# Optimization experiments

Hardware: AMD Instinct MI355X
Metric: run time of the kernel (lower is better)

The kernel has to match this reference:

```python
import jax, jax.numpy as jnp
import numpy as np

IMG_H = IMG_W = 640
NUM_CLASSES = 80
B = 8
NUM_ANCHORS = 76725
MAX_TOTAL = 200          # max_total_size == max_size_per_class
SCORE_TH = 0.5
IOU_TH = 0.5
K_CAND = 256             # per-class candidate pool for NMS (>= max survivors)
VARIANCES = jnp.asarray([0.1, 0.1, 0.2, 0.2], jnp.float32)


def _build_anchors(img_h, img_w):
    # RetinaNet AnchorBox: levels 3..7, 3 ratios x 3 scales, [cx, cy, w, h]
    ratios = [0.5, 1.0, 2.0]
    scales = [2.0 ** x for x in (0.0, 1.0 / 3.0, 2.0 / 3.0)]
    areas = [s * s for s in (32.0, 64.0, 128.0, 256.0, 512.0)]
    out = []
    for lvl, stride in enumerate([2 ** i for i in range(3, 8)]):
        dims = []
        for r in ratios:
            h = np.sqrt(areas[lvl] / r)
            w = areas[lvl] / h
            for s in scales:
                dims.append([w * s, h * s])
        dims = np.asarray(dims, np.float32)                      # [9,2]
        fh = int(np.ceil(img_h / stride)); fw = int(np.ceil(img_w / stride))
        rx = (np.arange(fw, dtype=np.float32) + 0.5) * stride
        ry = (np.arange(fh, dtype=np.float32) + 0.5) * stride
        cx, cy = np.meshgrid(rx, ry)
        centers = np.broadcast_to(np.stack([cx, cy], -1)[:, :, None, :], (fh, fw, 9, 2))
        d = np.broadcast_to(dims[None, None], (fh, fw, 9, 2))
        out.append(np.concatenate([centers, d], -1).reshape(-1, 4))
    return jnp.asarray(np.concatenate(out, 0))                   # [A,4]


def setup_inputs() -> dict:
    key = jax.random.key(0)
    k1, k2 = jax.random.split(key)
    box_pred = jax.random.normal(k1, (B, NUM_ANCHORS, 4), jnp.float32)
    cls_pred = jax.random.normal(k2, (B, NUM_ANCHORS, NUM_CLASSES), jnp.float32)
    anchor_boxes = _build_anchors(IMG_H, IMG_W)
    return {"box_pred": box_pred, "cls_pred": cls_pred, "anchor_boxes": anchor_boxes}


def _iou_one_vs_many(box, boxes):
    # box [4] vs boxes [K,4] in corner format
    lt = jnp.maximum(box[:2], boxes[:, :2])
    rb = jnp.minimum(box[2:], boxes[:, 2:])
    wh = jnp.maximum(rb - lt, 0.0)
    inter = wh[:, 0] * wh[:, 1]
    a1 = (box[2] - box[0]) * (box[3] - box[1])
    a2 = (boxes[:, 2] - boxes[:, 0]) * (boxes[:, 3] - boxes[:, 1])
    return inter / jnp.maximum(a1 + a2 - inter, 1e-8)


def _nms_keep(boxes, scores):
    # boxes [K,4] already sorted by descending score; greedy NMS
    eligible = scores > SCORE_TH
    idx = jnp.arange(K_CAND)

    def body(i, keep):
        iou = _iou_one_vs_many(boxes[i], boxes)
        suppress = (iou > IOU_TH) & (idx > i)
        return jnp.where(keep[i], keep & ~suppress, keep)

    keep = jax.lax.fori_loop(0, K_CAND, body, eligible)
    keep = keep & ((jnp.cumsum(keep) - 1) < MAX_TOTAL)           # max_size_per_class cap
    return keep


def _decode_and_nms(box_pred, cls_pred, anchor_boxes):
    scores_all = jax.nn.sigmoid(cls_pred)                        # [B,A,C]
    # decode: (dx,dy,dw,dh)*variances against [cx,cy,w,h] anchors
    d = box_pred * VARIANCES
    xy = d[..., :2] * anchor_boxes[None, :, 2:] + anchor_boxes[None, :, :2]
    wh = jnp.exp(d[..., 2:]) * anchor_boxes[None, :, 2:]
    boxes = jnp.concatenate([xy - 0.5 * wh, xy + 0.5 * wh], -1)  # [B,A,4] corners

    sc = jnp.swapaxes(scores_all, 1, 2)                          # [B,C,A]
    top_sc, top_idx = jax.lax.top_k(sc, K_CAND)                  # [B,C,K] sorted desc
    cand_boxes = jnp.take_along_axis(boxes[:, None], top_idx[..., None], axis=2)  # [B,C,K,4]

    keep = jax.lax.stop_gradient(jax.vmap(jax.vmap(_nms_keep))(cand_boxes, top_sc))  # [B,C,K]
    sel = jnp.where(keep, top_sc, -1.0)

    flat_sc = sel.reshape(B, -1)                                 # [B,C*K]
    flat_boxes = cand_boxes.reshape(B, -1, 4)
    flat_lbl = jnp.broadcast_to(jnp.arange(NUM_CLASSES)[None, :, None],
                                (B, NUM_CLASSES, K_CAND)).reshape(B, -1)

    fs, fi = jax.lax.top_k(flat_sc, MAX_TOTAL)                   # combine across classes
    out_boxes = jnp.take_along_axis(flat_boxes, fi[..., None], axis=1)
    out_lbl = jnp.take_along_axis(flat_lbl, fi, axis=1).astype(jnp.float32)
    valid = fs > 0.0                                             # pad invalid slots
    return (jnp.where(valid[..., None], out_boxes, 0.0),
            jnp.where(valid, fs, 0.0),
            jnp.where(valid, out_lbl, -1.0))


def reference(box_pred, cls_pred, anchor_boxes):
    return _decode_and_nms(box_pred, cls_pred, anchor_boxes)
```

## Files before the change

### kernel.cpp

```cpp
#include <hip/hip_runtime.h>
#include <math.h>
#include <stdint.h>

typedef unsigned long long u64;
typedef unsigned int u32;

#define NB 8
#define NA 76725
#define NC 80
#define KC 256
#define MAXT 200
#define CAP 2048
#define TCAP 1024
#define SELCAP 768
#define TAU 2.0f
#define TAU_STORE 2.5f
#define CHUNK 512
#define NCHUNK 150
#define BCAP 32
#define CSTRIDE 16

#define OFF_BUFA      0ull
#define OFF_CLASSLIST 5242880ull
#define OFF_CANDBOX   6553600ull
#define OFF_COUNTS    9175040ull

__device__ __forceinline__ void kf_proc(float4 v, int i, int a0,
                                        u64 (*bucket)[BCAP], u32* bcnt) {
  int a = a0 + i / (NC / 4);
  int c0 = (i % (NC / 4)) * 4;
  float vv[4] = {v.x, v.y, v.z, v.w};
#pragma unroll
  for (int j = 0; j < 4; j++) {
    if (vv[j] > TAU_STORE) {
      int c = c0 + j;
      u32 pos = atomicAdd(&bcnt[c], 1u);
      if (pos < BCAP)
        bucket[c][pos] = ((u64)__float_as_uint(vv[j]) << 32) | (u32)a;
    }
  }
}

__global__ __launch_bounds__(256) void kfilter(const float* __restrict__ cls,
                                               u64* __restrict__ bufA,
                                               u32* __restrict__ counts) {
  __shared__ u64 bucket[NC][BCAP];
  __shared__ u32 bcnt[NC];
  __shared__ u32 gbase[NC];
  __shared__ u32 pref[NC + 1];

  const int b = blockIdx.x / NCHUNK;
  const int ch = blockIdx.x % NCHUNK;
  const int tid = threadIdx.x;
  const int a0 = ch * CHUNK;
  const int aN = (NA - a0) < CHUNK ? (NA - a0) : CHUNK;

  for (int i = tid; i < NC; i += 256) bcnt[i] = 0;
  __syncthreads();

  const float4* p = (const float4*)(cls + ((size_t)b * NA + a0) * NC);
  const int n4 = aN * (NC / 4);
  for (int i0 = tid; i0 < n4; i0 += 2048) {
    float4 v[8];
    bool g[8];
#pragma unroll
    for (int u = 0; u < 8; u++) {
      g[u] = (i0 + u * 256) < n4;
      if (g[u]) v[u] = p[i0 + u * 256];
    }
#pragma unroll
    for (int u = 0; u < 8; u++)
      if (g[u]) kf_proc(v[u], i0 + u * 256, a0, bucket, bcnt);
  }
  __syncthreads();
  if (tid < NC) {
    u32 n = bcnt[tid];
    if (n > BCAP) n = BCAP;
    bcnt[tid] = n;
    gbase[tid] = atomicAdd(&counts[(b * NC + tid) * CSTRIDE], n);
  }
  __syncthreads();
  if (tid == 0) {
    u32 s = 0;
    for (int c = 0; c < NC; c++) { pref[c] = s; s += bcnt[c]; }
    pref[NC] = s;
  }
  __syncthreads();
  const int total = (int)pref[NC];
  for (int e = tid; e < total; e += 256) {
    int lo = 0, hi = NC;
    while (lo + 1 < hi) { int mid = (lo + hi) >> 1; if ((int)pref[mid] <= e) lo = mid; else hi = mid; }
    int c = lo;
    int loc = e - (int)pref[c];
    u32 gb = gbase[c] + (u32)loc;
    if (gb < TCAP)
      bufA[((size_t)(b * NC + c)) * TCAP + gb] = bucket[c][loc];
  }
}

__device__ __forceinline__ int logit_bin(u64 k) {
  float f = __uint_as_float((u32)(k >> 32));
  int bin = (int)(f * 170.0f);
  return bin < 0 ? 0 : (bin > 1023 ? 1023 : bin);
}

__device__ __forceinline__ bool iou_gt(float4 bi, float ai, float4 bj, float aj) {
  float lx = fmaxf(bi.x, bj.x), ly = fmaxf(bi.y, bj.y);
  float rx = fminf(bi.z, bj.z), ry = fminf(bi.w, bj.w);
  float wx = fmaxf(__fsub_rn(rx, lx), 0.0f);
  float wy = fmaxf(__fsub_rn(ry, ly), 0.0f);
  float inter = __fmul_rn(wx, wy);
  float uni = fmaxf(__fsub_rn(__fadd_rn(ai, aj), inter), 1e-8f);
  return __fdiv_rn(inter, uni) > 0.5f;
}

__global__ __launch_bounds__(256) void kselect(
    const float* __restrict__ cls, const float* __restrict__ boxp,
    const float* __restrict__ anc, const u64* __restrict__ bufA,
    const u32* __restrict__ counts, u64* __restrict__ classList,
    float4* __restrict__ candBox) {
  __shared__ __align__(16) char smem[24576];
  u64* sbuf = (u64*)smem;
  u64 (*scolT)[KC] = (u64(*)[KC])smem;
  float4* sBox = (float4*)(smem + 8192);
  float* sAr = (float*)(smem + 12288);
  u32* hist = (u32*)(smem + 16384);
  u64* sel = (u64*)(smem + 16384);
  u64* skey = (u64*)(smem + 22528);
  __shared__ u32 sRowAnyLo[4], sRowAnyHi[4];
  __shared__ int sNsel, sExtra, sSb;

  const int tid = threadIdx.x;
  const int bc = blockIdx.x;
  const int b = bc / NC, c = bc % NC;
  const u64* buf = bufA + (size_t)bc * TCAP;

  int cntT = (int)counts[bc * CSTRIDE];
  if (cntT > TCAP) cntT = TCAP;

  for (int i = tid; i < 1024; i += 256) hist[i] = 0;
  if (tid == 0) { sNsel = 0; sExtra = 0; }
  skey[tid] = 0;

  int cnt;
  if (cntT >= KC) {
    cnt = cntT;
    for (int e = tid; e < cnt; e += 256) sbuf[e] = buf[e];
  } else {
    __syncthreads();
    for (int a = tid; a < NA; a += 256) {
      float x = cls[((size_t)b * NA + a) * NC + c];
      if (x > TAU) {
        int pos = atomicAdd(&sExtra, 1);
        if (pos < CAP) sbuf[pos] = ((u64)__float_as_uint(x) << 32) | (u32)a;
      }
    }
    __syncthreads();
    if (sExtra < KC) {
      for (int a = tid; a < NA; a += 256) {
        float x = cls[((size_t)b * NA + a) * NC + c];
        if (x > 0.0f && !(x > TAU)) {
          int pos = atomicAdd(&sExtra, 1);
          if (pos < CAP) sbuf[pos] = ((u64)__float_as_uint(x) << 32) | (u32)a;
        }
      }
      __syncthreads();
    }
    cnt = sExtra < CAP ? sExtra : CAP;
  }
  __syncthreads();

  for (int e = tid; e < cnt; e += 256) atomicAdd(&hist[logit_bin(sbuf[e])], 1u);
  __syncthreads();

  if (tid < 64) {
    int s = 0;
#pragma unroll
    for (int i = 0; i < 16; i++) s += (int)hist[tid * 16 + i];
    int suf = s;
#pragma unroll
    for (int d = 1; d < 64; d <<= 1) {
      int t = __shfl_down(suf, d, 64);
      if (tid + d < 64) suf += t;
    }
    u64 mask = __ballot(suf >= KC);
    int sb = mask ? (63 - __clzll((long long)mask)) : 0;
    if (tid == 0) sSb = sb;
  }
  __syncthreads();
  const int sb = sSb;

  for (int e = tid; e < cnt; e += 256) {
    u64 k = sbuf[e];
    if ((logit_bin(k) >> 4) >= sb) {
      float f = __uint_as_float((u32)(k >> 32));
      float sc = 1.0f / (1.0f + expf(-f));
      int pos = atomicAdd(&sNsel, 1);
      if (pos < SELCAP)
        sel[pos] = ((u64)__float_as_uint(sc) << 32) | (0xFFFFFFFFu - (u32)k);
    }
  }
  __syncthreads();
  int nsel = sNsel;
  if (nsel > SELCAP) nsel = SELCAP;

#pragma unroll
  for (int w = 0; w < 4; w++) scolT[w][tid] = 0ull;
  for (int e = tid; e < nsel; e += 256) {
    u64 k = sel[e];
    int r = 0;
    int q = 0;
    const int nful = nsel & ~7;
    for (; q < nful; q += 8) {
      u64 t0 = sel[q],     t1 = sel[q + 1], t2 = sel[q + 2], t3 = sel[q + 3];
      u64 t4 = sel[q + 4], t5 = sel[q + 5], t6 = sel[q + 6], t7 = sel[q + 7];
      r += (t0 > k) + (t1 > k) + (t2 > k) + (t3 > k) +
           (t4 > k) + (t5 > k) + (t6 > k) + (t7 > k);
    }
    for (; q < nsel; q++) r += sel[q] > k;
    if (r < KC) skey[r] = k;
  }
  __syncthreads();

  {
    if (tid < 4) { sRowAnyLo[tid] = 0; sRowAnyHi[tid] = 0; }
    u64 k = skey[tid];
    u32 a = 0xFFFFFFFFu - (u32)k;
    if (k == 0ull || a >= NA) a = 0;
    float4 p = ((const float4*)boxp)[(size_t)b * NA + a];
    float4 an = ((const float4*)anc)[a];
    float dx = __fmul_rn(p.x, 0.1f), dy = __fmul_rn(p.y, 0.1f);
    float dw = __fmul_rn(p.z, 0.2f), dh = __fmul_rn(p.w, 0.2f);
    float cx = __fadd_rn(__fmul_rn(dx, an.z), an.x);
    float cy = __fadd_rn(__fmul_rn(dy, an.w), an.y);
    float w = __fmul_rn(expf(dw), an.z);
    float h = __fmul_rn(expf(dh), an.w);
    float4 bx;
    bx.x = __fsub_rn(cx, __fmul_rn(0.5f, w));
    bx.y = __fsub_rn(cy, __fmul_rn(0.5f, h));
    bx.z = __fadd_rn(cx, __fmul_rn(0.5f, w));
    bx.w = __fadd_rn(cy, __fmul_rn(0.5f, h));
    sBox[tid] = bx;
    sAr[tid] = __fmul_rn(__fsub_rn(bx.z, bx.x), __fsub_rn(bx.w, bx.y));
    candBox[(size_t)bc * KC + tid] = bx;
  }
  __syncthreads();

  {
    auto proc_seg = [&](int j, int ibeg, int iend) {
      float4 bj = sBox[j];
      float aj = sAr[j];
#pragma unroll
      for (int w = 0; w < 4; w++) {
        int lo = ibeg > (w << 6) ? ibeg : (w << 6);
        int hi = iend < ((w + 1) << 6) ? iend : ((w + 1) << 6);
        u64 bits = 0ull;
        int i = lo;
        for (; i + 3 < hi; i += 4) {
          float4 b0 = sBox[i], b1 = sBox[i + 1], b2 = sBox[i + 2], b3 = sBox[i + 3];
          float a0 = sAr[i], a1 = sAr[i + 1], a2 = sAr[i + 2], a3 = sAr[i + 3];
          bits |= (u64)iou_gt(b0, a0, bj, aj) << (i & 63);
          bits |= (u64)iou_gt(b1, a1, bj, aj) << ((i + 1) & 63);
          bits |= (u64)iou_gt(b2, a2, bj, aj) << ((i + 2) & 63);
          bits |= (u64)iou_gt(b3, a3, bj, aj) << ((i + 3) & 63);
        }
        for (; i < hi; i++)
          bits |= (u64)iou_gt(sBox[i], sAr[i], bj, aj) << (i & 63);
        if (bits) {
          u32* p = (u32*)&scolT[w][j];
          u32 blo = (u32)bits, bhi = (u32)(bits >> 32);
          if (blo) atomicOr(p, blo);
          if (bhi) atomicOr(p + 1, bhi);
        }
      }
    };
    const int u = tid & 127, h = tid >> 7;
    if (h == 0) {
      proc_seg(u, 0, u);
      proc_seg(255 - u, 0, 128 - u);
    } else {
      proc_seg(255 - u, 128 - u, 255 - u);
    }
  }
  __syncthreads();

  {
#pragma unroll
    for (int w = 0; w < 4; w++) {
      u64 r = scolT[w][tid];
#pragma unroll
      for (int m = 1; m < 64; m <<= 1) {
        int rlo = __shfl_xor((int)(u32)r, m, 64);
        int rhi = __shfl_xor((int)(r >> 32), m, 64);
        r |= ((u64)(u32)rhi << 32) | (u32)rlo;
      }
      if ((tid & 63) == 0) {
        atomicOr(&sRowAnyLo[w], (u32)r);
        atomicOr(&sRowAnyHi[w], (u32)(r >> 32));
      }
    }
  }
  __syncthreads();

  if (tid < 64) {
    const int ln = tid;
    u64 C[4][4];
#pragma unroll
    for (int s = 0; s < 4; s++)
#pragma unroll
      for (int w = 0; w < 4; w++) C[s][w] = scolT[w][s * 64 + ln];
    int keep = 0;
#pragma unroll
    for (int s = 0; s < 4; s++)
      if (skey[s * 64 + ln] != 0ull) keep |= (1 << s);
#pragma unroll
    for (int w = 0; w < 4; w++) {
      u64 c0 = C[0][w], c1 = C[1][w], c2 = C[2][w], c3 = C[3][w];
      u64 rw = ((u64)sRowAnyHi[w] << 32) | (u64)sRowAnyLo[w];
      while (rw) {
        int t = __builtin_ctzll(rw);
        rw &= rw - 1;
        int kt = __shfl(keep, t, 64);
        if ((kt >> w) & 1) {
          int sup = (int)((c0 >> t) & 1) | ((int)((c1 >> t) & 1) << 1) |
                    ((int)((c2 >> t) & 1) << 2) | ((int)((c3 >> t) & 1) << 3);
          keep &= ~sup;
        }
      }
    }
    u64 m[4];
#pragma unroll
    for (int s = 0; s < 4; s++) m[s] = __ballot((keep >> s) & 1);
    int tot = 0;
#pragma unroll
    for (int s = 0; s < 4; s++) tot += __popcll(m[s]);
    int keptTotal = tot < MAXT ? tot : MAXT;
    u64 lmask = (1ull << ln) - 1ull;
    int base = 0;
#pragma unroll
    for (int s = 0; s < 4; s++) {
      int j = s * 64 + ln;
      int cum = base + (int)__popcll(m[s] & lmask);
      if (((keep >> s) & 1) && cum < MAXT) {
        u64 hi = skey[j] >> 32;
        classList[(size_t)bc * KC + cum] =
            (hi << 32) | (u64)(0xFFFFFFFFu - (u32)(c * KC + j));
      }
      base += (int)__popcll(m[s]);
    }
    for (int t2 = ln; t2 < KC; t2 += 64)
      if (t2 >= keptTotal) classList[(size_t)bc * KC + t2] = 0;
  }
}

__device__ __forceinline__ u64 shfl64(u64 v, int src) {
  int lo = __shfl((int)(u32)v, src, 64);
  int hi = __shfl((int)(v >> 32), src, 64);
  return ((u64)(u32)hi << 32) | (u32)lo;
}
__device__ __forceinline__ u64 shflxor64(u64 v, int mask) {
  int lo = __shfl_xor((int)(u32)v, mask, 64);
  int hi = __shfl_xor((int)(v >> 32), mask, 64);
  return ((u64)(u32)hi << 32) | (u32)lo;
}
#define CSWAP(a, b) { if ((a) < (b)) { u64 _t = (a); (a) = (b); (b) = _t; } }

__device__ __forceinline__ void wave_merge(u64 acc[4], const u64 cur[4], int ln) {
  u64 t0 = shfl64(cur[3], 63 - ln);
  u64 t1 = shfl64(cur[2], 63 - ln);
  u64 t2 = shfl64(cur[1], 63 - ln);
  u64 t3 = shfl64(cur[0], 63 - ln);
  acc[0] = acc[0] > t0 ? acc[0] : t0;
  acc[1] = acc[1] > t1 ? acc[1] : t1;
  acc[2] = acc[2] > t2 ? acc[2] : t2;
  acc[3] = acc[3] > t3 ? acc[3] : t3;
  CSWAP(acc[0], acc[2]); CSWAP(acc[1], acc[3]);
  CSWAP(acc[0], acc[1]); CSWAP(acc[2], acc[3]);
#pragma unroll
  for (int s = 32; s >= 1; s >>= 1) {
#pragma unroll
    for (int k = 0; k < 4; k++) {
      u64 o = shflxor64(acc[k], s);
      u64 mx = acc[k] > o ? acc[k] : o;
      u64 mn = acc[k] < o ? acc[k] : o;
      acc[k] = ((ln & s) == 0) ? mx : mn;
    }
  }
}

__global__ __launch_bounds__(256) void kmerge(const u64* __restrict__ classList,
                                              const float4* __restrict__ candBox,
                                              float* __restrict__ out) {
  __shared__ u64 lds[4 * KC];
  const int tid = threadIdx.x, b = blockIdx.x;
  const int w = tid >> 6, ln = tid & 63;
  const u64* base = classList + ((size_t)b * NC + w * 20) * KC;
  u64 acc[4];
#pragma unroll
  for (int k = 0; k < 4; k++) acc[k] = base[k * 64 + ln];
  for (int m = 1; m < 20; m++) {
    u64 cur[4];
#pragma unroll
    for (int k = 0; k < 4; k++) cur[k] = base[(size_t)m * KC + k * 64 + ln];
    wave_merge(acc, cur, ln);
  }
#pragma unroll
  for (int k = 0; k < 4; k++) lds[w * KC + k * 64 + ln] = acc[k];
  __syncthreads();
  if (w == 0) {
    for (int m = 1; m < 4; m++) {
      u64 cur[4];
#pragma unroll
      for (int k = 0; k < 4; k++) cur[k] = lds[m * KC + k * 64 + ln];
      wave_merge(acc, cur, ln);
    }
#pragma unroll
    for (int k = 0; k < 4; k++) lds[k * 64 + ln] = acc[k];
  }
  __syncthreads();
  if (tid < MAXT) {
    u64 k = lds[tid];
    float4 bx = make_float4(0.f, 0.f, 0.f, 0.f);
    float sc = 0.0f, lb = -1.0f;
    if (k != 0ull) {
      sc = __uint_as_float((u32)(k >> 32));
      u32 flat = 0xFFFFFFFFu - (u32)k;
      int cc = (int)(flat >> 8), kk = (int)(flat & 255u);
      bx = candBox[((size_t)b * NC + cc) * KC + kk];
      lb = (float)cc;
    }
    float* ob = out + ((size_t)b * MAXT + tid) * 4;
    ob[0] = bx.x; ob[1] = bx.y; ob[2] = bx.z; ob[3] = bx.w;
    out[NB * MAXT * 4 + b * MAXT + tid] = sc;
    out[NB * MAXT * 4 + NB * MAXT + b * MAXT + tid] = lb;
  }
}

extern "C" void kernel_launch(void* const* d_in, const int* in_sizes, int n_in,
                              void* d_out, int out_size, void* d_ws,
                              size_t ws_size, hipStream_t stream) {
  const float* boxp = (const float*)d_in[0];
  const float* cls = (const float*)d_in[1];
  const float* anc = (const float*)d_in[2];
  char* ws = (char*)d_ws;
  u64* bufA = (u64*)(ws + OFF_BUFA);
  u64* classList = (u64*)(ws + OFF_CLASSLIST);
  float4* candBox = (float4*)(ws + OFF_CANDBOX);
  u32* counts = (u32*)(ws + OFF_COUNTS);

  hipMemsetAsync(counts, 0, NB * NC * CSTRIDE * sizeof(u32), stream);
  kfilter<<<NB * NCHUNK, 256, 0, stream>>>(cls, bufA, counts);
  kselect<<<NB * NC, 256, 0, stream>>>(cls, boxp, anc, bufA, counts, classList,
                                       candBox);
  kmerge<<<NB, 256, 0, stream>>>(classList, candBox, (float*)d_out);
}
```

Measured before the change: 358.7 us.

## Store sigmoid keys at filter time and drop histogram preselection in kselect

```diff
diff --git a/kernel.cpp b/kernel.cpp
--- a/kernel.cpp
+++ b/kernel.cpp
@@ -10,9 +10,7 @@
 #define NC 80
 #define KC 256
 #define MAXT 200
-#define CAP 2048
 #define TCAP 1024
-#define SELCAP 768
 #define TAU 2.0f
 #define TAU_STORE 2.5f
 #define CHUNK 512
@@ -25,6 +23,11 @@
 #define OFF_CANDBOX   6553600ull
 #define OFF_COUNTS    9175040ull
 
+__device__ __forceinline__ u64 make_key(float f, u32 a) {
+  float sc = 1.0f / (1.0f + expf(-f));
+  return ((u64)__float_as_uint(sc) << 32) | (0xFFFFFFFFu - a);
+}
+
 __device__ __forceinline__ void kf_proc(float4 v, int i, int a0,
                                         u64 (*bucket)[BCAP], u32* bcnt) {
   int a = a0 + i / (NC / 4);
@@ -36,7 +39,7 @@
       int c = c0 + j;
       u32 pos = atomicAdd(&bcnt[c], 1u);
       if (pos < BCAP)
-        bucket[c][pos] = ((u64)__float_as_uint(vv[j]) << 32) | (u32)a;
+        bucket[c][pos] = make_key(vv[j], (u32)a);
     }
   }
 }
@@ -98,12 +101,6 @@
   }
 }
 
-__device__ __forceinline__ int logit_bin(u64 k) {
-  float f = __uint_as_float((u32)(k >> 32));
-  int bin = (int)(f * 170.0f);
-  return bin < 0 ? 0 : (bin > 1023 ? 1023 : bin);
-}
-
 __device__ __forceinline__ bool iou_gt(float4 bi, float ai, float4 bj, float aj) {
   float lx = fmaxf(bi.x, bj.x), ly = fmaxf(bi.y, bj.y);
   float rx = fminf(bi.z, bj.z), ry = fminf(bi.w, bj.w);
@@ -119,16 +116,13 @@
     const float* __restrict__ anc, const u64* __restrict__ bufA,
     const u32* __restrict__ counts, u64* __restrict__ classList,
     float4* __restrict__ candBox) {
-  __shared__ __align__(16) char smem[24576];
-  u64* sbuf = (u64*)smem;
+  __shared__ __align__(16) char smem[15360];
+  u64* sel = (u64*)smem;
   u64 (*scolT)[KC] = (u64(*)[KC])smem;
   float4* sBox = (float4*)(smem + 8192);
   float* sAr = (float*)(smem + 12288);
-  u32* hist = (u32*)(smem + 16384);
-  u64* sel = (u64*)(smem + 16384);
-  u64* skey = (u64*)(smem + 22528);
-  __shared__ u32 sRowAnyLo[4], sRowAnyHi[4];
-  __shared__ int sNsel, sExtra, sSb;
+  u64* skey = (u64*)(smem + 13312);
+  __shared__ int sExtra;
 
   const int tid = threadIdx.x;
   const int bc = blockIdx.x;
@@ -138,21 +132,26 @@
   int cntT = (int)counts[bc * CSTRIDE];
   if (cntT > TCAP) cntT = TCAP;
 
-  for (int i = tid; i < 1024; i += 256) hist[i] = 0;
-  if (tid == 0) { sNsel = 0; sExtra = 0; }
-  skey[tid] = 0;
-
   int cnt;
   if (cntT >= KC) {
     cnt = cntT;
-    for (int e = tid; e < cnt; e += 256) sbuf[e] = buf[e];
+    u64 v0 = 0, v1 = 0, v2 = 0, v3 = 0;
+    if (tid < cnt) v0 = buf[tid];
+    if (tid + 256 < cnt) v1 = buf[tid + 256];
+    if (tid + 512 < cnt) v2 = buf[tid + 512];
+    if (tid + 768 < cnt) v3 = buf[tid + 768];
+    if (tid < cnt) sel[tid] = v0;
+    if (tid + 256 < cnt) sel[tid + 256] = v1;
+    if (tid + 512 < cnt) sel[tid + 512] = v2;
+    if (tid + 768 < cnt) sel[tid + 768] = v3;
   } else {
+    if (tid == 0) sExtra = 0;
     __syncthreads();
     for (int a = tid; a < NA; a += 256) {
       float x = cls[((size_t)b * NA + a) * NC + c];
       if (x > TAU) {
         int pos = atomicAdd(&sExtra, 1);
-        if (pos < CAP) sbuf[pos] = ((u64)__float_as_uint(x) << 32) | (u32)a;
+        if (pos < TCAP) sel[pos] = make_key(x, (u32)a);
       }
     }
     __syncthreads();
@@ -161,69 +160,58 @@
         float x = cls[((size_t)b * NA + a) * NC + c];
         if (x > 0.0f && !(x > TAU)) {
           int pos = atomicAdd(&sExtra, 1);
-          if (pos < CAP) sbuf[pos] = ((u64)__float_as_uint(x) << 32) | (u32)a;
+          if (pos < TCAP) sel[pos] = make_key(x, (u32)a);
         }
       }
       __syncthreads();
     }
-    cnt = sExtra < CAP ? sExtra : CAP;
-  }
-  __syncthreads();
-
-  for (int e = tid; e < cnt; e += 256) atomicAdd(&hist[logit_bin(sbuf[e])], 1u);
-  __syncthreads();
-
-  if (tid < 64) {
-    int s = 0;
-#pragma unroll
-    for (int i = 0; i < 16; i++) s += (int)hist[tid * 16 + i];
-    int suf = s;
-#pragma unroll
-    for (int d = 1; d < 64; d <<= 1) {
-      int t = __shfl_down(suf, d, 64);
-      if (tid + d < 64) suf += t;
-    }
-    u64 mask = __ballot(suf >= KC);
-    int sb = mask ? (63 - __clzll((long long)mask)) : 0;
-    if (tid == 0) sSb = sb;
-  }
-  __syncthreads();
-  const int sb = sSb;
-
-  for (int e = tid; e < cnt; e += 256) {
-    u64 k = sbuf[e];
-    if ((logit_bin(k) >> 4) >= sb) {
-      float f = __uint_as_float((u32)(k >> 32));
-      float sc = 1.0f / (1.0f + expf(-f));
-      int pos = atomicAdd(&sNsel, 1);
-      if (pos < SELCAP)
-        sel[pos] = ((u64)__float_as_uint(sc) << 32) | (0xFFFFFFFFu - (u32)k);
-    }
-  }
-  __syncthreads();
-  int nsel = sNsel;
-  if (nsel > SELCAP) nsel = SELCAP;
-
-#pragma unroll
-  for (int w = 0; w < 4; w++) scolT[w][tid] = 0ull;
-  for (int e = tid; e < nsel; e += 256) {
-    u64 k = sel[e];
-    int r = 0;
+    cnt = sExtra < TCAP ? sExtra : TCAP;
+  }
+  skey[tid] = 0;
+  __syncthreads();
+
+  {
+    const bool has1 = cnt > 256, has2 = cnt > 512, has3 = cnt > 768;
+    u64 k0 = (tid < cnt) ? sel[tid] : 0;
+    u64 k1 = has1 && (tid + 256 < cnt) ? sel[tid + 256] : 0;
+    u64 k2 = has2 && (tid + 512 < cnt) ? sel[tid + 512] : 0;
+    u64 k3 = has3 && (tid + 768 < cnt) ? sel[tid + 768] : 0;
+    int r0 = 0, r1 = 0, r2 = 0, r3 = 0;
     int q = 0;
-    const int nful = nsel & ~7;
+    const int nful = cnt & ~7;
     for (; q < nful; q += 8) {
       u64 t0 = sel[q],     t1 = sel[q + 1], t2 = sel[q + 2], t3 = sel[q + 3];
       u64 t4 = sel[q + 4], t5 = sel[q + 5], t6 = sel[q + 6], t7 = sel[q + 7];
-      r += (t0 > k) + (t1 > k) + (t2 > k) + (t3 > k) +
-           (t4 > k) + (t5 > k) + (t6 > k) + (t7 > k);
-    }
-    for (; q < nsel; q++) r += sel[q] > k;
-    if (r < KC) skey[r] = k;
+      r0 += (t0 > k0) + (t1 > k0) + (t2 > k0) + (t3 > k0) +
+            (t4 > k0) + (t5 > k0) + (t6 > k0) + (t7 > k0);
+      if (has1)
+        r1 += (t0 > k1) + (t1 > k1) + (t2 > k1) + (t3 > k1) +
+              (t4 > k1) + (t5 > k1) + (t6 > k1) + (t7 > k1);
+      if (has2)
+        r2 += (t0 > k2) + (t1 > k2) + (t2 > k2) + (t3 > k2) +
+              (t4 > k2) + (t5 > k2) + (t6 > k2) + (t7 > k2);
+      if (has3)
+        r3 += (t0 > k3) + (t1 > k3) + (t2 > k3) + (t3 > k3) +
+              (t4 > k3) + (t5 > k3) + (t6 > k3) + (t7 > k3);
+    }
+    for (; q < cnt; q++) {
+      u64 t = sel[q];
+      r0 += (t > k0);
+      if (has1) r1 += (t > k1);
+      if (has2) r2 += (t > k2);
+      if (has3) r3 += (t > k3);
+    }
+    __syncthreads();
+    if (tid < cnt && r0 < KC) skey[r0] = k0;
+    if (has1 && tid + 256 < cnt && r1 < KC) skey[r1] = k1;
+    if (has2 && tid + 512 < cnt && r2 < KC) skey[r2] = k2;
+    if (has3 && tid + 768 < cnt && r3 < KC) skey[r3] = k3;
   }
   __syncthreads();
 
   {
-    if (tid < 4) { sRowAnyLo[tid] = 0; sRowAnyHi[tid] = 0; }
+#pragma unroll
+    for (int w = 0; w < 4; w++) scolT[w][tid] = 0ull;
     u64 k = skey[tid];
     u32 a = 0xFFFFFFFFu - (u32)k;
     if (k == 0ull || a >= NA) a = 0;
@@ -284,24 +272,6 @@
   }
   __syncthreads();
 
-  {
-#pragma unroll
-    for (int w = 0; w < 4; w++) {
-      u64 r = scolT[w][tid];
-#pragma unroll
-      for (int m = 1; m < 64; m <<= 1) {
-        int rlo = __shfl_xor((int)(u32)r, m, 64);
-        int rhi = __shfl_xor((int)(r >> 32), m, 64);
-        r |= ((u64)(u32)rhi << 32) | (u32)rlo;
-      }
-      if ((tid & 63) == 0) {
-        atomicOr(&sRowAnyLo[w], (u32)r);
-        atomicOr(&sRowAnyHi[w], (u32)(r >> 32));
-      }
-    }
-  }
-  __syncthreads();
-
   if (tid < 64) {
     const int ln = tid;
     u64 C[4][4];
@@ -316,7 +286,13 @@
 #pragma unroll
     for (int w = 0; w < 4; w++) {
       u64 c0 = C[0][w], c1 = C[1][w], c2 = C[2][w], c3 = C[3][w];
-      u64 rw = ((u64)sRowAnyHi[w] << 32) | (u64)sRowAnyLo[w];
+      u64 rw = c0 | c1 | c2 | c3;
+#pragma unroll
+      for (int m = 1; m < 64; m <<= 1) {
+        int rlo = __shfl_xor((int)(u32)rw, m, 64);
+        int rhi = __shfl_xor((int)(rw >> 32), m, 64);
+        rw |= ((u64)(u32)rhi << 32) | (u32)rlo;
+      }
       while (rw) {
         int t = __builtin_ctzll(rw);
         rw &= rw - 1;
```

Result: slower. 367.7 us (+2.5%).
